# Kernel tuning notes

Measured on AMD Instinct MI355X. Metric: run time of the kernel, lower is better.

## Reference

```python
import jax, jax.numpy as jnp
import numpy as np

B, N, D_IN, D_OUT, H = 2, 2048, 1024, 1024, 16
HD = D_OUT // H


def setup_inputs() -> dict:
    key = jax.random.key(0)
    ks = jax.random.split(key, 6)
    s_in = 1.0 / np.sqrt(D_IN)
    s_out = 1.0 / np.sqrt(D_OUT)
    return {
        "x": jax.random.normal(ks[0], (B, N, D_IN), dtype=jnp.float32),
        "Wq": jax.random.uniform(ks[1], (D_IN, D_OUT), jnp.float32, -s_in, s_in),
        "Wk": jax.random.uniform(ks[2], (D_IN, D_OUT), jnp.float32, -s_in, s_in),
        "Wv": jax.random.uniform(ks[3], (D_IN, D_OUT), jnp.float32, -s_in, s_in),
        "Wo": jax.random.uniform(ks[4], (D_OUT, D_OUT), jnp.float32, -s_out, s_out),
        "bo": jax.random.uniform(ks[5], (D_OUT,), jnp.float32, -s_out, s_out),
    }


def reference(x, Wq, Wk, Wv, Wo, bo):
    b, n, _ = x.shape
    # project and split heads: [b, n, d_out] -> [b, h, n, hd]
    def heads(w):
        return w.reshape(b, n, H, HD).transpose(0, 2, 1, 3)
    q = heads(x @ Wq)
    k = heads(x @ Wk)
    v = heads(x @ Wv)
    # materialized causal attention (dropout rate 0.0 -> identity)
    scores = jnp.einsum("bhqd,bhkd->bhqk", q, k)
    causal = jnp.tril(jnp.ones((n, n), dtype=bool))  # keep lower triangle
    scores = jnp.where(causal, scores, -jnp.inf)
    attn = jax.nn.softmax(scores / np.sqrt(HD), axis=-1)
    ctx = jnp.einsum("bhqk,bhkd->bhqd", attn, v)
    ctx = ctx.transpose(0, 2, 1, 3).reshape(b, n, D_OUT)
    return ctx @ Wo + bo
```

## Files before the change

### kernel.cpp

```cpp
#include <hip/hip_runtime.h>
#include <math.h>
#include <stdint.h>

#define B_ 2
#define N_ 2048
#define D_ 1024
#define H_ 16
#define HD_ 64
#define M_ (B_ * N_)

typedef __bf16 bf16x8 __attribute__((ext_vector_type(8)));
typedef float f32x4 __attribute__((ext_vector_type(4)));

__device__ __forceinline__ ushort bfbits(float f) {
    __bf16 h = (__bf16)f;
    return __builtin_bit_cast(ushort, h);
}

__device__ __forceinline__ void glds16(const ushort* g, ushort* l) {
    __builtin_amdgcn_global_load_lds(
        (const __attribute__((address_space(1))) uint32_t*)g,
        (__attribute__((address_space(3))) uint32_t*)l, 16, 0, 0);
}

__global__ __launch_bounds__(256) void cvt_x(const float* __restrict__ x,
                                             ushort* __restrict__ xb) {
    int i = blockIdx.x * 256 + threadIdx.x;
    float4 v = ((const float4*)x)[i];
    ushort4 o;
    o.x = bfbits(v.x); o.y = bfbits(v.y); o.z = bfbits(v.z); o.w = bfbits(v.w);
    ((ushort4*)xb)[i] = o;
}

__global__ __launch_bounds__(256) void cvt_w(const float* __restrict__ W0,
                                             const float* __restrict__ W1,
                                             const float* __restrict__ W2,
                                             const float* __restrict__ W3,
                                             ushort* __restrict__ Wt) {
    __shared__ float T[32][33];
    const float* W = (blockIdx.z == 0) ? W0 : (blockIdx.z == 1) ? W1
                   : (blockIdx.z == 2) ? W2 : W3;
    ushort* out = Wt + (size_t)blockIdx.z * D_ * D_;
    const int t = threadIdx.x;
    const int k0 = blockIdx.x * 32, n0 = blockIdx.y * 32;
    {
        int kl = t >> 3, nl = (t & 7) * 4;
        float4 v = *(const float4*)&W[(size_t)(k0 + kl) * D_ + n0 + nl];
        T[kl][nl] = v.x; T[kl][nl + 1] = v.y; T[kl][nl + 2] = v.z; T[kl][nl + 3] = v.w;
    }
    __syncthreads();
    {
        int nl = t >> 3, k4 = (t & 7) * 4;
        ushort4 o;
        o.x = bfbits(T[k4 + 0][nl]); o.y = bfbits(T[k4 + 1][nl]);
        o.z = bfbits(T[k4 + 2][nl]); o.w = bfbits(T[k4 + 3][nl]);
        *(ushort4*)&out[(size_t)(n0 + nl) * D_ + k0 + k4] = o;
    }
}

__global__ __launch_bounds__(256) void transp_v(const ushort* __restrict__ vb,
                                                ushort* __restrict__ vt) {
    __shared__ ushort T[64][72];
    const int t = threadIdx.x;
    const int nt = blockIdx.x, bh = blockIdx.y;
    const ushort* src = vb + ((size_t)bh * N_ + nt * 64) * HD_;
    #pragma unroll
    for (int it = 0; it < 2; ++it) {
        int fi = it * 256 + t;
        int r = fi >> 3, c = (fi & 7) * 8;
        *(uint4*)&T[r][c] = *(const uint4*)&src[(size_t)r * HD_ + c];
    }
    __syncthreads();
    ushort* dst = vt + (size_t)bh * HD_ * N_ + nt * 64;
    #pragma unroll
    for (int it = 0; it < 2; ++it) {
        int fi = it * 256 + t;
        int hd = fi >> 3, n0 = (fi & 7) * 8;
        uint4 o;
        o.x = (uint32_t)T[n0 + 0][hd] | ((uint32_t)T[n0 + 1][hd] << 16);
        o.y = (uint32_t)T[n0 + 2][hd] | ((uint32_t)T[n0 + 3][hd] << 16);
        o.z = (uint32_t)T[n0 + 4][hd] | ((uint32_t)T[n0 + 5][hd] << 16);
        o.w = (uint32_t)T[n0 + 6][hd] | ((uint32_t)T[n0 + 7][hd] << 16);
        *(uint4*)&dst[(size_t)hd * N_ + n0] = o;
    }
}

#define BK 32

__device__ __forceinline__ void gemm_tile(const ushort* __restrict__ A,
                                          const ushort* __restrict__ Bt,
                                          int K, int tileM, int tileN,
                                          ushort* As, ushort* Bs,
                                          f32x4 acc[4][4]) {
    const int t = threadIdx.x;
    const int l = t & 63;
    const int w = __builtin_amdgcn_readfirstlane(t >> 6);
    const int wr = w >> 1, wc = w & 1;
    const int li = l & 15, lg = l >> 4;
    const int lr = l >> 2;
    const int colu = (((l & 3) ^ (lr & 3)) << 3);
    const int swz = (li & 3) << 3;

    for (int k0 = 0; k0 < K; k0 += BK) {
        __syncthreads();
        #pragma unroll
        for (int it = 0; it < 2; ++it) {
            const int c2 = it * 4 + w;
            const int row = c2 * 16 + lr;
            glds16(&A[(size_t)(tileM + row) * K + k0 + colu], &As[c2 * 512]);
            glds16(&Bt[(size_t)(tileN + row) * K + k0 + colu], &Bs[c2 * 512]);
        }
        __syncthreads();
        bf16x8 a[4], b[4];
        #pragma unroll
        for (int m = 0; m < 4; ++m)
            a[m] = *(const bf16x8*)&As[(wr * 64 + m * 16 + li) * 32 + ((lg << 3) ^ swz)];
        #pragma unroll
        for (int n = 0; n < 4; ++n)
            b[n] = *(const bf16x8*)&Bs[(wc * 64 + n * 16 + li) * 32 + ((lg << 3) ^ swz)];
        #pragma unroll
        for (int m = 0; m < 4; ++m)
            #pragma unroll
            for (int n = 0; n < 4; ++n)
                acc[m][n] = __builtin_amdgcn_mfma_f32_16x16x32_bf16(a[m], b[n], acc[m][n], 0, 0, 0);
    }
}

#define QSCALE 0.180336880f

__global__ __launch_bounds__(256) void qkv_gemm(const ushort* __restrict__ xb,
                                                const ushort* __restrict__ Wt,
                                                ushort* __restrict__ q,
                                                ushort* __restrict__ k,
                                                ushort* __restrict__ v) {
    __shared__ ushort As[128 * 32];
    __shared__ ushort Bs[128 * 32];
    f32x4 acc[4][4];
    #pragma unroll
    for (int m = 0; m < 4; ++m)
        #pragma unroll
        for (int n = 0; n < 4; ++n)
            acc[m][n] = (f32x4){0.f, 0.f, 0.f, 0.f};

    const int tileM = blockIdx.x * 128;
    const int wsel = blockIdx.y >> 3;
    const int tileN = (blockIdx.y & 7) * 128;
    const ushort* Bmat = Wt + (size_t)wsel * D_ * D_;

    gemm_tile(xb, Bmat, D_, tileM, tileN, As, Bs, acc);

    ushort* out = (wsel == 0) ? q : (wsel == 1) ? k : v;
    const float scale = (wsel == 0) ? QSCALE : 1.0f;
    const int l = threadIdx.x & 63, w = threadIdx.x >> 6;
    const int wr = w >> 1, wc = w & 1;
    const int li = l & 15, lg = l >> 4;
    #pragma unroll
    for (int m = 0; m < 4; ++m)
        #pragma unroll
        for (int n = 0; n < 4; ++n)
            #pragma unroll
            for (int r = 0; r < 4; ++r) {
                int grow = tileM + wr * 64 + m * 16 + lg * 4 + r;
                int gcol = tileN + wc * 64 + n * 16 + li;
                int b = grow >> 11, nn = grow & (N_ - 1);
                int h = gcol >> 6, hd = gcol & 63;
                out[((size_t)(b * H_ + h) * N_ + nn) * HD_ + hd] = bfbits(acc[m][n][r] * scale);
            }
}

__global__ __launch_bounds__(256) void out_gemm(const ushort* __restrict__ ctx,
                                                const ushort* __restrict__ Wt,
                                                const float* __restrict__ bo,
                                                float* __restrict__ outp) {
    __shared__ ushort As[128 * 32];
    __shared__ ushort Bs[128 * 32];
    f32x4 acc[4][4];
    #pragma unroll
    for (int m = 0; m < 4; ++m)
        #pragma unroll
        for (int n = 0; n < 4; ++n)
            acc[m][n] = (f32x4){0.f, 0.f, 0.f, 0.f};

    const int tileM = blockIdx.x * 128;
    const int tileN = blockIdx.y * 128;
    const ushort* Bmat = Wt + (size_t)3 * D_ * D_;

    gemm_tile(ctx, Bmat, D_, tileM, tileN, As, Bs, acc);

    const int l = threadIdx.x & 63, w = threadIdx.x >> 6;
    const int wr = w >> 1, wc = w & 1;
    const int li = l & 15, lg = l >> 4;
    #pragma unroll
    for (int n = 0; n < 4; ++n) {
        float bias = bo[tileN + wc * 64 + n * 16 + li];
        #pragma unroll
        for (int m = 0; m < 4; ++m)
            #pragma unroll
            for (int r = 0; r < 4; ++r) {
                int grow = tileM + wr * 64 + m * 16 + lg * 4 + r;
                int gcol = tileN + wc * 64 + n * 16 + li;
                outp[(size_t)grow * D_ + gcol] = acc[m][n][r] + bias;
            }
    }
}

__global__ __launch_bounds__(256) void attn_fwd(const ushort* __restrict__ q,
                                                const ushort* __restrict__ k,
                                                const ushort* __restrict__ vt,
                                                ushort* __restrict__ ctx) {
    __shared__ ushort Ks[2][64 * 64];
    __shared__ ushort Vs[2][64 * 64];
    __shared__ ushort Ps[4][16][72];

    const int t = threadIdx.x;
    const int l = t & 63;
    const int w = __builtin_amdgcn_readfirstlane(t >> 6);
    const int li = l & 15, lg = l >> 4;
    const int f = blockIdx.x;
    const int bh = ((f & 7) << 2) | ((f >> 3) & 3);
    const int pj = f >> 5;

    const ushort* Qg = q + (size_t)bh * N_ * HD_;
    const ushort* Kg = k + (size_t)bh * N_ * HD_;
    const ushort* Vg = vt + (size_t)bh * HD_ * N_;
    const int b = bh >> 4, h = bh & 15;

    const int r8 = l >> 3;
    const int soff = ((l & 7) ^ r8) * 8;
    const int rswz = li & 7;

    for (int task = 0; task < 2; ++task) {
        const int qt = (task == 0) ? pj : 31 - pj;
        const int nkb = qt + 1;
        const int qb64 = qt * 64 + w * 16;
        const int qg = qb64 + li;

        bf16x8 bq[2];
        #pragma unroll
        for (int tk = 0; tk < 2; ++tk)
            bq[tk] = *(const bf16x8*)&Qg[(size_t)qg * HD_ + tk * 32 + lg * 8];

        f32x4 od[4];
        #pragma unroll
        for (int db = 0; db < 4; ++db) od[db] = (f32x4){0.f, 0.f, 0.f, 0.f};
        float mrun = -INFINITY, lsum = 0.f;

        #pragma unroll
        for (int i = 0; i < 2; ++i) {
            const int seg = w + i * 4;
            const int row = seg * 8 + r8;
            glds16(&Kg[(size_t)row * HD_ + soff], &Ks[0][seg * 512]);
            glds16(&Vg[(size_t)row * N_ + soff], &Vs[0][seg * 512]);
        }
        __syncthreads();

        int cur = 0;
        for (int kb = 0; kb < nkb; ++kb) {
            if (kb + 1 < nkb) {
                #pragma unroll
                for (int i = 0; i < 2; ++i) {
                    const int seg = w + i * 4;
                    const int row = seg * 8 + r8;
                    glds16(&Kg[(size_t)((kb + 1) * 64 + row) * HD_ + soff], &Ks[cur ^ 1][seg * 512]);
                    glds16(&Vg[(size_t)row * N_ + (kb + 1) * 64 + soff], &Vs[cur ^ 1][seg * 512]);
                }
            }

            f32x4 st[4];
            #pragma unroll
            for (int c = 0; c < 4; ++c) {
                st[c] = (f32x4){0.f, 0.f, 0.f, 0.f};
                #pragma unroll
                for (int tk = 0; tk < 2; ++tk) {
                    bf16x8 kf = *(const bf16x8*)&Ks[cur][(c * 16 + li) * 64 + (((tk * 4 + lg) ^ rswz) * 8)];
                    st[c] = __builtin_amdgcn_mfma_f32_16x16x32_bf16(kf, bq[tk], st[c], 0, 0, 0);
                }
            }

            const bool lastkb = (kb == qt);
            float sv[4][4];
            #pragma unroll
            for (int c = 0; c < 4; ++c)
                #pragma unroll
                for (int r = 0; r < 4; ++r) {
                    const int kgl = kb * 64 + c * 16 + lg * 4 + r;
                    sv[c][r] = (lastkb && kgl > qg) ? -INFINITY : st[c][r];
                }

            float mx = fmaxf(fmaxf(sv[0][0], sv[0][1]), fmaxf(sv[0][2], sv[0][3]));
            #pragma unroll
            for (int c = 1; c < 4; ++c)
                mx = fmaxf(mx, fmaxf(fmaxf(sv[c][0], sv[c][1]), fmaxf(sv[c][2], sv[c][3])));
            mx = fmaxf(mx, __shfl_xor(mx, 16));
            mx = fmaxf(mx, __shfl_xor(mx, 32));

            if (!__all(mx - mrun <= 8.f)) {
                const float mn = fmaxf(mrun, mx);
                const float al = exp2f(mrun - mn);
                lsum *= al;
                mrun = mn;
                float ar[4];
                #pragma unroll
                for (int r = 0; r < 4; ++r) ar[r] = __shfl(al, lg * 4 + r);
                #pragma unroll
                for (int db = 0; db < 4; ++db)
                    #pragma unroll
                    for (int r = 0; r < 4; ++r) od[db][r] *= ar[r];
            }

            float rs = 0.f;
            #pragma unroll
            for (int c = 0; c < 4; ++c) {
                float p0 = exp2f(sv[c][0] - mrun);
                float p1 = exp2f(sv[c][1] - mrun);
                float p2 = exp2f(sv[c][2] - mrun);
                float p3 = exp2f(sv[c][3] - mrun);
                rs += (p0 + p1) + (p2 + p3);
                uint2 pk;
                pk.x = (uint32_t)bfbits(p0) | ((uint32_t)bfbits(p1) << 16);
                pk.y = (uint32_t)bfbits(p2) | ((uint32_t)bfbits(p3) << 16);
                *(uint2*)&Ps[w][li][c * 16 + lg * 4] = pk;
            }
            rs += __shfl_xor(rs, 16);
            rs += __shfl_xor(rs, 32);
            lsum += rs;

            #pragma unroll
            for (int tj = 0; tj < 2; ++tj) {
                bf16x8 pa = *(const bf16x8*)&Ps[w][li][tj * 32 + lg * 8];
                #pragma unroll
                for (int db = 0; db < 4; ++db) {
                    bf16x8 bv = *(const bf16x8*)&Vs[cur][(db * 16 + li) * 64 + (((tj * 4 + lg) ^ rswz) * 8)];
                    od[db] = __builtin_amdgcn_mfma_f32_16x16x32_bf16(pa, bv, od[db], 0, 0, 0);
                }
            }

            __syncthreads();
            cur ^= 1;
        }

        #pragma unroll
        for (int r = 0; r < 4; ++r) {
            const float inv = 1.f / __shfl(lsum, lg * 4 + r);
            const int grow = qb64 + lg * 4 + r;
            #pragma unroll
            for (int db = 0; db < 4; ++db)
                ctx[((size_t)(b * N_ + grow)) * D_ + h * 64 + db * 16 + li] = bfbits(od[db][r] * inv);
        }
    }
}

extern "C" void kernel_launch(void* const* d_in, const int* in_sizes, int n_in,
                              void* d_out, int out_size, void* d_ws, size_t ws_size,
                              hipStream_t stream) {
    (void)in_sizes; (void)n_in; (void)out_size; (void)ws_size;
    const float* x  = (const float*)d_in[0];
    const float* Wq = (const float*)d_in[1];
    const float* Wk = (const float*)d_in[2];
    const float* Wv = (const float*)d_in[3];
    const float* Wo = (const float*)d_in[4];
    const float* bo = (const float*)d_in[5];
    float* outp = (float*)d_out;

    ushort* xb  = (ushort*)d_ws;
    ushort* Wt  = xb + (size_t)M_ * D_;
    ushort* qb  = Wt + (size_t)4 * D_ * D_;
    ushort* kb  = qb + (size_t)B_ * H_ * N_ * HD_;
    ushort* vb  = kb + (size_t)B_ * H_ * N_ * HD_;
    ushort* vtb = vb + (size_t)B_ * H_ * N_ * HD_;
    ushort* ctx = vtb + (size_t)B_ * H_ * N_ * HD_;

    cvt_x<<<dim3((M_ * D_ / 4) / 256), 256, 0, stream>>>(x, xb);
    cvt_w<<<dim3(32, 32, 4), 256, 0, stream>>>(Wq, Wk, Wv, Wo, Wt);
    qkv_gemm<<<dim3(32, 24), 256, 0, stream>>>(xb, Wt, qb, kb, vb);
    transp_v<<<dim3(32, 32), 256, 0, stream>>>(vb, vtb);
    attn_fwd<<<dim3(512), 256, 0, stream>>>(qb, kb, vtb, ctx);
    out_gemm<<<dim3(32, 8), 256, 0, stream>>>(ctx, Wt, bo, outp);
}
```

Measured before the change: 124.2 us.

## Stage GEMM epilogues through LDS, pipeline QK with softmax-PV, one q-tile per block

The QKV and output GEMM epilogues now stage results through shared memory so global stores become coalesced 16-byte row writes, and Q/K/V are kept in row-major [B*N, D] layout instead of a per-head layout. The attention kernel is restructured into a software pipeline that computes QK scores for the next key block while doing softmax and PV on the current one, with a triple-buffered V tile. It also launches one block per query tile instead of pairing tiles, and uses packed bf16 conversion instructions. The extra LDS and synchronisation lower occupancy, and dropping tile pairing may leave the causal workload imbalanced across blocks.

```diff
diff --git a/kernel.cpp b/kernel.cpp
--- a/kernel.cpp
+++ b/kernel.cpp
@@ -63,12 +63,13 @@
     __shared__ ushort T[64][72];
     const int t = threadIdx.x;
     const int nt = blockIdx.x, bh = blockIdx.y;
-    const ushort* src = vb + ((size_t)bh * N_ + nt * 64) * HD_;
+    const int b = bh >> 4, h = bh & 15;
+    const ushort* src = vb + ((size_t)(b * N_ + nt * 64)) * D_ + h * 64;
     #pragma unroll
     for (int it = 0; it < 2; ++it) {
         int fi = it * 256 + t;
         int r = fi >> 3, c = (fi & 7) * 8;
-        *(uint4*)&T[r][c] = *(const uint4*)&src[(size_t)r * HD_ + c];
+        *(uint4*)&T[r][c] = *(const uint4*)&src[(size_t)r * D_ + c];
     }
     __syncthreads();
     ushort* dst = vt + (size_t)bh * HD_ * N_ + nt * 64;
@@ -135,6 +136,7 @@
                                                 ushort* __restrict__ v) {
     __shared__ ushort As[128 * 32];
     __shared__ ushort Bs[128 * 32];
+    __shared__ ushort Eps[32][136];
     f32x4 acc[4][4];
     #pragma unroll
     for (int m = 0; m < 4; ++m)
@@ -151,21 +153,28 @@
 
     ushort* out = (wsel == 0) ? q : (wsel == 1) ? k : v;
     const float scale = (wsel == 0) ? QSCALE : 1.0f;
-    const int l = threadIdx.x & 63, w = threadIdx.x >> 6;
+    const int t = threadIdx.x;
+    const int l = t & 63, w = t >> 6;
     const int wr = w >> 1, wc = w & 1;
     const int li = l & 15, lg = l >> 4;
-    #pragma unroll
-    for (int m = 0; m < 4; ++m)
+    const int lrow = t & 31;
+    const int coff = (t >> 5) * 16;
+
+    #pragma unroll
+    for (int m = 0; m < 4; ++m) {
+        __syncthreads();
         #pragma unroll
         for (int n = 0; n < 4; ++n)
             #pragma unroll
-            for (int r = 0; r < 4; ++r) {
-                int grow = tileM + wr * 64 + m * 16 + lg * 4 + r;
-                int gcol = tileN + wc * 64 + n * 16 + li;
-                int b = grow >> 11, nn = grow & (N_ - 1);
-                int h = gcol >> 6, hd = gcol & 63;
-                out[((size_t)(b * H_ + h) * N_ + nn) * HD_ + hd] = bfbits(acc[m][n][r] * scale);
-            }
+            for (int r = 0; r < 4; ++r)
+                Eps[wr * 16 + lg * 4 + r][wc * 64 + n * 16 + li] = bfbits(acc[m][n][r] * scale);
+        __syncthreads();
+        const int grow = tileM + (lrow >> 4) * 64 + m * 16 + (lrow & 15);
+        uint4 v0 = *(const uint4*)&Eps[lrow][coff];
+        uint4 v1 = *(const uint4*)&Eps[lrow][coff + 8];
+        *(uint4*)&out[(size_t)grow * D_ + tileN + coff] = v0;
+        *(uint4*)&out[(size_t)grow * D_ + tileN + coff + 8] = v1;
+    }
 }
 
 __global__ __launch_bounds__(256) void out_gemm(const ushort* __restrict__ ctx,
@@ -174,6 +183,7 @@
                                                 float* __restrict__ outp) {
     __shared__ ushort As[128 * 32];
     __shared__ ushort Bs[128 * 32];
+    __shared__ float Epf[32][132];
     f32x4 acc[4][4];
     #pragma unroll
     for (int m = 0; m < 4; ++m)
@@ -187,20 +197,108 @@
 
     gemm_tile(ctx, Bmat, D_, tileM, tileN, As, Bs, acc);
 
-    const int l = threadIdx.x & 63, w = threadIdx.x >> 6;
+    const int t = threadIdx.x;
+    const int l = t & 63, w = t >> 6;
     const int wr = w >> 1, wc = w & 1;
     const int li = l & 15, lg = l >> 4;
-    #pragma unroll
-    for (int n = 0; n < 4; ++n) {
-        float bias = bo[tileN + wc * 64 + n * 16 + li];
-        #pragma unroll
-        for (int m = 0; m < 4; ++m)
+    const int lrow = t & 31;
+    const int coff = (t >> 5) * 16;
+
+    float bias[4];
+    #pragma unroll
+    for (int n = 0; n < 4; ++n) bias[n] = bo[tileN + wc * 64 + n * 16 + li];
+
+    #pragma unroll
+    for (int m = 0; m < 4; ++m) {
+        __syncthreads();
+        #pragma unroll
+        for (int n = 0; n < 4; ++n)
+            #pragma unroll
+            for (int r = 0; r < 4; ++r)
+                Epf[wr * 16 + lg * 4 + r][wc * 64 + n * 16 + li] = acc[m][n][r] + bias[n];
+        __syncthreads();
+        const int grow = tileM + (lrow >> 4) * 64 + m * 16 + (lrow & 15);
+        #pragma unroll
+        for (int j = 0; j < 4; ++j) {
+            float4 vv = *(const float4*)&Epf[lrow][coff + j * 4];
+            *(float4*)&outp[(size_t)grow * D_ + tileN + coff + j * 4] = vv;
+        }
+    }
+}
+
+__device__ __forceinline__ void qk_mfma(f32x4 st[4], const ushort* Kb,
+                                        const bf16x8 bq[2],
+                                        int li, int lg, int rswz) {
+    #pragma unroll
+    for (int c = 0; c < 4; ++c) {
+        st[c] = (f32x4){0.f, 0.f, 0.f, 0.f};
+        #pragma unroll
+        for (int tk = 0; tk < 2; ++tk) {
+            bf16x8 kf = *(const bf16x8*)&Kb[(c * 16 + li) * 64 + (((tk * 4 + lg) ^ rswz) * 8)];
+            st[c] = __builtin_amdgcn_mfma_f32_16x16x32_bf16(kf, bq[tk], st[c], 0, 0, 0);
+        }
+    }
+}
+
+__device__ __forceinline__ void softmax_pv(f32x4 st[4], const ushort* Vb,
+                                           bool masked, int jkb, int qg,
+                                           int li, int lg, int rswz,
+                                           ushort* PsW,
+                                           float& mrun, float& lsum,
+                                           f32x4 od[4]) {
+    if (masked) {
+        #pragma unroll
+        for (int c = 0; c < 4; ++c)
             #pragma unroll
             for (int r = 0; r < 4; ++r) {
-                int grow = tileM + wr * 64 + m * 16 + lg * 4 + r;
-                int gcol = tileN + wc * 64 + n * 16 + li;
-                outp[(size_t)grow * D_ + gcol] = acc[m][n][r] + bias;
+                const int kgl = jkb * 64 + c * 16 + lg * 4 + r;
+                if (kgl > qg) st[c][r] = -INFINITY;
             }
+    }
+    float mx = fmaxf(fmaxf(st[0][0], st[0][1]), fmaxf(st[0][2], st[0][3]));
+    #pragma unroll
+    for (int c = 1; c < 4; ++c)
+        mx = fmaxf(mx, fmaxf(fmaxf(st[c][0], st[c][1]), fmaxf(st[c][2], st[c][3])));
+    mx = fmaxf(mx, __shfl_xor(mx, 16));
+    mx = fmaxf(mx, __shfl_xor(mx, 32));
+    if (!__all(mx - mrun <= 8.f)) {
+        const float mn = fmaxf(mrun, mx);
+        const float al = exp2f(mrun - mn);
+        lsum *= al;
+        mrun = mn;
+        float ar[4];
+        #pragma unroll
+        for (int r = 0; r < 4; ++r) ar[r] = __shfl(al, lg * 4 + r);
+        #pragma unroll
+        for (int db = 0; db < 4; ++db)
+            #pragma unroll
+            for (int r = 0; r < 4; ++r) od[db][r] *= ar[r];
+    }
+    float rs = 0.f;
+    #pragma unroll
+    for (int c = 0; c < 4; ++c) {
+        float p0 = exp2f(st[c][0] - mrun);
+        float p1 = exp2f(st[c][1] - mrun);
+        float p2 = exp2f(st[c][2] - mrun);
+        float p3 = exp2f(st[c][3] - mrun);
+        rs += (p0 + p1) + (p2 + p3);
+        uint32_t w0, w1;
+        asm("v_cvt_pk_bf16_f32 %0, %1, %2" : "=v"(w0) : "v"(p0), "v"(p1));
+        asm("v_cvt_pk_bf16_f32 %0, %1, %2" : "=v"(w1) : "v"(p2), "v"(p3));
+        uint2 pk; pk.x = w0; pk.y = w1;
+        *(uint2*)&PsW[li * 72 + c * 16 + lg * 4] = pk;
+    }
+    rs += __shfl_xor(rs, 16);
+    rs += __shfl_xor(rs, 32);
+    lsum += rs;
+    #pragma unroll
+    for (int tj = 0; tj < 2; ++tj) {
+        bf16x8 pa = *(const bf16x8*)&PsW[li * 72 + tj * 32 + lg * 8];
+        #pragma unroll
+        for (int db = 0; db < 4; ++db) {
+            bf16x8 bv = *(const bf16x8*)&Vb[(db * 16 + li) * 64 + (((tj * 4 + lg) ^ rswz) * 8)];
+            od[db] = __builtin_amdgcn_mfma_f32_16x16x32_bf16(pa, bv, od[db], 0, 0, 0);
+        }
     }
 }
 
@@ -208,8 +306,8 @@
                                                 const ushort* __restrict__ k,
                                                 const ushort* __restrict__ vt,
                                                 ushort* __restrict__ ctx) {
-    __shared__ ushort Ks[2][64 * 64];
-    __shared__ ushort Vs[2][64 * 64];
+    __shared__ ushort Ks[2][4096];
+    __shared__ ushort Vs[3][4096];
     __shared__ ushort Ps[4][16][72];
 
     const int t = threadIdx.x;
@@ -218,135 +316,83 @@
     const int li = l & 15, lg = l >> 4;
     const int f = blockIdx.x;
     const int bh = ((f & 7) << 2) | ((f >> 3) & 3);
-    const int pj = f >> 5;
-
-    const ushort* Qg = q + (size_t)bh * N_ * HD_;
-    const ushort* Kg = k + (size_t)bh * N_ * HD_;
+    const int qt = 31 - (f >> 5);
+    const int b = bh >> 4, h = bh & 15;
+
+    const ushort* Qg = q + ((size_t)b * N_) * D_ + h * 64;
+    const ushort* Kg = k + ((size_t)b * N_) * D_ + h * 64;
     const ushort* Vg = vt + (size_t)bh * HD_ * N_;
-    const int b = bh >> 4, h = bh & 15;
+    ushort* PsW = &Ps[w][0][0];
 
     const int r8 = l >> 3;
     const int soff = ((l & 7) ^ r8) * 8;
     const int rswz = li & 7;
 
-    for (int task = 0; task < 2; ++task) {
-        const int qt = (task == 0) ? pj : 31 - pj;
-        const int nkb = qt + 1;
-        const int qb64 = qt * 64 + w * 16;
-        const int qg = qb64 + li;
-
-        bf16x8 bq[2];
-        #pragma unroll
-        for (int tk = 0; tk < 2; ++tk)
-            bq[tk] = *(const bf16x8*)&Qg[(size_t)qg * HD_ + tk * 32 + lg * 8];
-
-        f32x4 od[4];
-        #pragma unroll
-        for (int db = 0; db < 4; ++db) od[db] = (f32x4){0.f, 0.f, 0.f, 0.f};
-        float mrun = -INFINITY, lsum = 0.f;
-
+    const int qb64 = qt * 64 + w * 16;
+    const int qg = qb64 + li;
+
+    bf16x8 bq[2];
+    #pragma unroll
+    for (int tk = 0; tk < 2; ++tk)
+        bq[tk] = *(const bf16x8*)&Qg[(size_t)qg * D_ + tk * 32 + lg * 8];
+
+    f32x4 od[4];
+    #pragma unroll
+    for (int db = 0; db < 4; ++db) od[db] = (f32x4){0.f, 0.f, 0.f, 0.f};
+    float mrun = -INFINITY, lsum = 0.f;
+
+    #pragma unroll
+    for (int i = 0; i < 2; ++i) {
+        const int seg = w + i * 4;
+        const int row = seg * 8 + r8;
+        glds16(&Kg[(size_t)row * D_ + soff], &Ks[0][seg * 512]);
+        glds16(&Vg[(size_t)row * N_ + soff], &Vs[0][seg * 512]);
+    }
+    __syncthreads();
+
+    f32x4 stp[4];
+    if (qt >= 1) {
         #pragma unroll
         for (int i = 0; i < 2; ++i) {
             const int seg = w + i * 4;
             const int row = seg * 8 + r8;
-            glds16(&Kg[(size_t)row * HD_ + soff], &Ks[0][seg * 512]);
-            glds16(&Vg[(size_t)row * N_ + soff], &Vs[0][seg * 512]);
-        }
-        __syncthreads();
-
-        int cur = 0;
-        for (int kb = 0; kb < nkb; ++kb) {
-            if (kb + 1 < nkb) {
-                #pragma unroll
-                for (int i = 0; i < 2; ++i) {
-                    const int seg = w + i * 4;
-                    const int row = seg * 8 + r8;
-                    glds16(&Kg[(size_t)((kb + 1) * 64 + row) * HD_ + soff], &Ks[cur ^ 1][seg * 512]);
-                    glds16(&Vg[(size_t)row * N_ + (kb + 1) * 64 + soff], &Vs[cur ^ 1][seg * 512]);
-                }
+            glds16(&Kg[(size_t)(64 + row) * D_ + soff], &Ks[1][seg * 512]);
+            glds16(&Vg[(size_t)row * N_ + 64 + soff], &Vs[1][seg * 512]);
+        }
+    }
+    qk_mfma(stp, Ks[0], bq, li, lg, rswz);
+    __syncthreads();
+
+    int vwr = 2;
+    int vrd = 0;
+    for (int i = 1; i <= qt; ++i) {
+        if (i + 1 <= qt) {
+            #pragma unroll
+            for (int ii = 0; ii < 2; ++ii) {
+                const int seg = w + ii * 4;
+                const int row = seg * 8 + r8;
+                glds16(&Kg[(size_t)((i + 1) * 64 + row) * D_ + soff], &Ks[(i + 1) & 1][seg * 512]);
+                glds16(&Vg[(size_t)row * N_ + (i + 1) * 64 + soff], &Vs[vwr][seg * 512]);
             }
-
-            f32x4 st[4];
-            #pragma unroll
-            for (int c = 0; c < 4; ++c) {
-                st[c] = (f32x4){0.f, 0.f, 0.f, 0.f};
-                #pragma unroll
-                for (int tk = 0; tk < 2; ++tk) {
-                    bf16x8 kf = *(const bf16x8*)&Ks[cur][(c * 16 + li) * 64 + (((tk * 4 + lg) ^ rswz) * 8)];
-                    st[c] = __builtin_amdgcn_mfma_f32_16x16x32_bf16(kf, bq[tk], st[c], 0, 0, 0);
-                }
-            }
-
-            const bool lastkb = (kb == qt);
-            float sv[4][4];
-            #pragma unroll
-            for (int c = 0; c < 4; ++c)
-                #pragma unroll
-                for (int r = 0; r < 4; ++r) {
-                    const int kgl = kb * 64 + c * 16 + lg * 4 + r;
-                    sv[c][r] = (lastkb && kgl > qg) ? -INFINITY : st[c][r];
-                }
-
-            float mx = fmaxf(fmaxf(sv[0][0], sv[0][1]), fmaxf(sv[0][2], sv[0][3]));
-            #pragma unroll
-            for (int c = 1; c < 4; ++c)
-                mx = fmaxf(mx, fmaxf(fmaxf(sv[c][0], sv[c][1]), fmaxf(sv[c][2], sv[c][3])));
-            mx = fmaxf(mx, __shfl_xor(mx, 16));
-            mx = fmaxf(mx, __shfl_xor(mx, 32));
-
-            if (!__all(mx - mrun <= 8.f)) {
-                const float mn = fmaxf(mrun, mx);
-                const float al = exp2f(mrun - mn);
-                lsum *= al;
-                mrun = mn;
-                float ar[4];
-                #pragma unroll
-                for (int r = 0; r < 4; ++r) ar[r] = __shfl(al, lg * 4 + r);
-                #pragma unroll
-                for (int db = 0; db < 4; ++db)
-                    #pragma unroll
-                    for (int r = 0; r < 4; ++r) od[db][r] *= ar[r];
-            }
-
-            float rs = 0.f;
-            #pragma unroll
-            for (int c = 0; c < 4; ++c) {
-                float p0 = exp2f(sv[c][0] - mrun);
-                float p1 = exp2f(sv[c][1] - mrun);
-                float p2 = exp2f(sv[c][2] - mrun);
-                float p3 = exp2f(sv[c][3] - mrun);
-                rs += (p0 + p1) + (p2 + p3);
-                uint2 pk;
-                pk.x = (uint32_t)bfbits(p0) | ((uint32_t)bfbits(p1) << 16);
-                pk.y = (uint32_t)bfbits(p2) | ((uint32_t)bfbits(p3) << 16);
-                *(uint2*)&Ps[w][li][c * 16 + lg * 4] = pk;
-            }
-            rs += __shfl_xor(rs, 16);
-            rs += __shfl_xor(rs, 32);
-            lsum += rs;
-
-            #pragma unroll
-            for (int tj = 0; tj < 2; ++tj) {
-                bf16x8 pa = *(const bf16x8*)&Ps[w][li][tj * 32 + lg * 8];
-                #pragma unroll
-                for (int db = 0; db < 4; ++db) {
-                    bf16x8 bv = *(const bf16x8*)&Vs[cur][(db * 16 + li) * 64 + (((tj * 4 + lg) ^ rswz) * 8)];
-                    od[db] = __builtin_amdgcn_mfma_f32_16x16x32_bf16(pa, bv, od[db], 0, 0, 0);
-                }
-            }
-
-            __syncthreads();
-            cur ^= 1;
-        }
-
-        #pragma unroll
-        for (int r = 0; r < 4; ++r) {
-            const float inv = 1.f / __shfl(lsum, lg * 4 + r);
-            const int grow = qb64 + lg * 4 + r;
-            #pragma unroll
-            for (int db = 0; db < 4; ++db)
-                ctx[((size_t)(b * N_ + grow)) * D_ + h * 64 + db * 16 + li] = bfbits(od[db][r] * inv);
-        }
+        }
+        f32x4 stc[4];
+        qk_mfma(stc, Ks[i & 1], bq, li, lg, rswz);
+        softmax_pv(stp, Vs[vrd], false, i - 1, qg, li, lg, rswz, PsW, mrun, lsum, od);
+        #pragma unroll
+        for (int c = 0; c < 4; ++c) stp[c] = stc[c];
+        __syncthreads();
+        vwr = (vwr == 2) ? 0 : vwr + 1;
+        vrd = (vrd == 2) ? 0 : vrd + 1;
+    }
+    softmax_pv(stp, Vs[vrd], true, qt, qg, li, lg, rswz, PsW, mrun, lsum, od);
+
+    #pragma unroll
+    for (int r = 0; r < 4; ++r) {
+        const float inv = 1.f / __shfl(lsum, lg * 4 + r);
+        const int grow = qb64 + lg * 4 + r;
+        #pragma unroll
+        for (int db = 0; db < 4; ++db)
+            ctx[((size_t)(b * N_ + grow)) * D_ + h * 64 + db * 16 + li] = bfbits(od[db][r] * inv);
     }
 }
 
@@ -365,15 +411,15 @@
     ushort* xb  = (ushort*)d_ws;
     ushort* Wt  = xb + (size_t)M_ * D_;
     ushort* qb  = Wt + (size_t)4 * D_ * D_;
-    ushort* kb  = qb + (size_t)B_ * H_ * N_ * HD_;
-    ushort* vb  = kb + (size_t)B_ * H_ * N_ * HD_;
-    ushort* vtb = vb + (size_t)B_ * H_ * N_ * HD_;
-    ushort* ctx = vtb + (size_t)B_ * H_ * N_ * HD_;
+    ushort* kb  = qb + (size_t)M_ * D_;
+    ushort* vb  = kb + (size_t)M_ * D_;
+    ushort* vtb = vb + (size_t)M_ * D_;
+    ushort* ctx = vtb + (size_t)M_ * D_;
 
     cvt_x<<<dim3((M_ * D_ / 4) / 256), 256, 0, stream>>>(x, xb);
     cvt_w<<<dim3(32, 32, 4), 256, 0, stream>>>(Wq, Wk, Wv, Wo, Wt);
     qkv_gemm<<<dim3(32, 24), 256, 0, stream>>>(xb, Wt, qb, kb, vb);
     transp_v<<<dim3(32, 32), 256, 0, stream>>>(vb, vtb);
-    attn_fwd<<<dim3(512), 256, 0, stream>>>(qb, kb, vtb, ctx);
+    attn_fwd<<<dim3(1024), 256, 0, stream>>>(qb, kb, vtb, ctx);
     out_gemm<<<dim3(32, 8), 256, 0, stream>>>(ctx, Wt, bo, outp);
 }
```

Measured after the change: 123.8 us. About the same (-0.3%).
